# Kernel tuning notes

Measured on AMD Instinct MI355X. Metric: run time of the kernel, lower is better.

The kernel has to match this reference:

```python
import jax, jax.numpy as jnp
import numpy as np

NUM_HEADS = 12


def setup_inputs() -> dict:
    key = jax.random.key(0)
    k1, k2, k3 = jax.random.split(key, 3)
    B, N, C = 4, 2048, 768
    x = jax.random.normal(k1, (B, N, C), dtype=jnp.float32)
    # Linear weights stored as [in, out] so y = x @ W (+ b); matches torch Linear math.
    w_qkv = jax.random.normal(k2, (C, 3 * C), dtype=jnp.float32) * (C ** -0.5)
    w_proj = jax.random.normal(k3, (C, C), dtype=jnp.float32) * (C ** -0.5)
    b_proj = jnp.zeros((C,), dtype=jnp.float32)
    return {"x": x, "w_qkv": w_qkv, "w_proj": w_proj, "b_proj": b_proj}


def reference(x, w_qkv, w_proj, b_proj):
    B, N, C = x.shape
    H = NUM_HEADS
    D = C // H
    scale = D ** -0.5
    qkv = (x @ w_qkv).reshape(B, N, 3, H, D)
    qkv = jnp.transpose(qkv, (2, 0, 3, 1, 4))  # [3, B, H, N, D]
    q, k, v = qkv[0], qkv[1], qkv[2]
    attn = jnp.einsum("bhnd,bhmd->bhnm", q, k) * scale  # [B, H, N, N]
    # causal mask (triu with offset 1), filled with -finfo.max as in the torch code
    causal_mask = jnp.triu(jnp.ones((N, N), dtype=bool), k=1)
    mask_value = -jnp.finfo(attn.dtype).max
    attn = jnp.where(causal_mask, mask_value, attn)
    attn = jax.nn.softmax(attn, axis=-1)
    attn = jnp.nan_to_num(attn)
    out = jnp.einsum("bhnm,bhmd->bhnd", attn, v)  # [B, H, N, D]
    out = jnp.transpose(out, (0, 2, 1, 3)).reshape(B, N, C)
    return out @ w_proj + b_proj
```

## Files before the change

### kernel.cpp

```cpp
#include <hip/hip_runtime.h>
#include <hip/hip_bf16.h>
#include <math.h>

#define BATCH 4
#define SEQ   2048
#define CDIM  768
#define NHEAD 12
#define HDIM  64
#define MROWS (BATCH*SEQ)
#define QKVC  (3*CDIM)

typedef __bf16    bf16x8 __attribute__((ext_vector_type(8)));
typedef _Float16  f16x8  __attribute__((ext_vector_type(8)));
typedef _Float16  f16x4  __attribute__((ext_vector_type(4)));
typedef float     f32x4  __attribute__((ext_vector_type(4)));

__device__ __forceinline__ void async16(const void* g, void* l) {
  __builtin_amdgcn_global_load_lds(
      (const __attribute__((address_space(1))) void*)g,
      (__attribute__((address_space(3))) void*)l, 16, 0, 0);
}

__global__ __launch_bounds__(256) void cast_f32_bf16(
    const float* __restrict__ in, __bf16* __restrict__ out, int n8) {
  int i = blockIdx.x * 256 + threadIdx.x;
  if (i >= n8) return;
  float4 a = reinterpret_cast<const float4*>(in)[i * 2];
  float4 b = reinterpret_cast<const float4*>(in)[i * 2 + 1];
  bf16x8 o;
  o[0] = (__bf16)a.x; o[1] = (__bf16)a.y; o[2] = (__bf16)a.z; o[3] = (__bf16)a.w;
  o[4] = (__bf16)b.x; o[5] = (__bf16)b.y; o[6] = (__bf16)b.z; o[7] = (__bf16)b.w;
  reinterpret_cast<bf16x8*>(out)[i] = o;
}

__global__ __launch_bounds__(256) void transpose_cast(
    const float* __restrict__ w, __bf16* __restrict__ wt, int K, int N) {
  __shared__ float sh[32][33];
  const int n0 = blockIdx.x * 32, k0 = blockIdx.y * 32;
  const int tx = threadIdx.x, ty = threadIdx.y;
#pragma unroll
  for (int i = 0; i < 4; ++i)
    sh[ty + i * 8][tx] = w[(size_t)(k0 + ty + i * 8) * N + n0 + tx];
  __syncthreads();
#pragma unroll
  for (int i = 0; i < 4; ++i)
    wt[(size_t)(n0 + ty + i * 8) * K + k0 + tx] = (__bf16)sh[tx][ty + i * 8];
}

__global__ __launch_bounds__(256) void transpose_v(
    const __bf16* __restrict__ qkv, _Float16* __restrict__ vT) {
  __shared__ float sh[32][33];
  const int c0 = blockIdx.x * 32;
  const int m0 = blockIdx.y * 32;
  const int tx = threadIdx.x, ty = threadIdx.y;
#pragma unroll
  for (int i = 0; i < 4; ++i)
    sh[ty + i * 8][tx] =
        (float)qkv[(size_t)(m0 + ty + i * 8) * QKVC + 2 * CDIM + c0 + tx];
  __syncthreads();
#pragma unroll
  for (int i = 0; i < 4; ++i)
    vT[(size_t)(c0 + ty + i * 8) * MROWS + m0 + tx] = (_Float16)sh[tx][ty + i * 8];
}

template <bool BF16OUT>
__global__ __launch_bounds__(256) void gemm_bf16_kernel(
    const __bf16* __restrict__ A, const __bf16* __restrict__ Bt,
    const float* __restrict__ bias, void* __restrict__ Cout,
    int M, int N, int K) {
  __shared__ __align__(16) __bf16 As[128 * 32];
  __shared__ __align__(16) __bf16 Bs[128 * 32];
  const int tid  = threadIdx.x;
  const int w    = tid >> 6;
  const int lane = tid & 63;
  const int quad = lane >> 4;
  const int lr   = lane & 15;
  const int wr   = w >> 1, wc = w & 1;
  const int mBase = blockIdx.y * 128, nBase = blockIdx.x * 128;

  f32x4 acc[4][4] = {};

  const int srow = lane >> 2;
  const int sk8  = (lane & 3) * 8;
  const __bf16* aSrc0 = A  + (size_t)(mBase + w * 32 + srow) * K + sk8;
  const __bf16* aSrc1 = aSrc0 + (size_t)16 * K;
  const __bf16* bSrc0 = Bt + (size_t)(nBase + w * 32 + srow) * K + sk8;
  const __bf16* bSrc1 = bSrc0 + (size_t)16 * K;
  __bf16* aDst0 = &As[(w * 32 + 0) * 32];
  __bf16* aDst1 = &As[(w * 32 + 16) * 32];
  __bf16* bDst0 = &Bs[(w * 32 + 0) * 32];
  __bf16* bDst1 = &Bs[(w * 32 + 16) * 32];

  for (int k0 = 0; k0 < K; k0 += 32) {
    __syncthreads();
    async16(aSrc0 + k0, aDst0);
    async16(aSrc1 + k0, aDst1);
    async16(bSrc0 + k0, bDst0);
    async16(bSrc1 + k0, bDst1);
    __syncthreads();

    bf16x8 af[4], bfr[4];
#pragma unroll
    for (int mt = 0; mt < 4; ++mt)
      af[mt] = *reinterpret_cast<const bf16x8*>(
          &As[(wr * 64 + mt * 16 + lr) * 32 + quad * 8]);
#pragma unroll
    for (int nt = 0; nt < 4; ++nt)
      bfr[nt] = *reinterpret_cast<const bf16x8*>(
          &Bs[(wc * 64 + nt * 16 + lr) * 32 + quad * 8]);
#pragma unroll
    for (int mt = 0; mt < 4; ++mt)
#pragma unroll
      for (int nt = 0; nt < 4; ++nt)
        acc[mt][nt] = __builtin_amdgcn_mfma_f32_16x16x32_bf16(
            af[mt], bfr[nt], acc[mt][nt], 0, 0, 0);
  }

#pragma unroll
  for (int mt = 0; mt < 4; ++mt) {
#pragma unroll
    for (int nt = 0; nt < 4; ++nt) {
      const int col = nBase + wc * 64 + nt * 16 + lr;
#pragma unroll
      for (int r = 0; r < 4; ++r) {
        const size_t row = (size_t)(mBase + wr * 64 + mt * 16 + quad * 4 + r);
        if (BF16OUT) {
          ((__bf16*)Cout)[row * N + col] = (__bf16)acc[mt][nt][r];
        } else {
          ((float*)Cout)[row * N + col] = acc[mt][nt][r] + bias[col];
        }
      }
    }
  }
}

__global__ __launch_bounds__(256) void flash_mfma_kernel(
    const __bf16* __restrict__ qkv, const _Float16* __restrict__ vT,
    __bf16* __restrict__ out) {
  const int bid = blockIdx.x;
  const int iq  = 31 - (bid / (NHEAD * BATCH));
  const int hb  = bid % (NHEAD * BATCH);
  const int h   = hb % NHEAD;
  const int b   = hb / NHEAD;

  const int tid  = threadIdx.x;
  const int w    = tid >> 6;
  const int lane = tid & 63;
  const int quad = lane >> 4;
  const int lr   = lane & 15;

  __shared__ __align__(16) __bf16   Kf[2][4096];
  __shared__ __align__(16) _Float16 Vf[2][4096];

  bf16x8 qf[2];
  {
    const int qrow = iq * 64 + w * 16 + lr;
    const __bf16* qp = qkv + (size_t)(b * SEQ + qrow) * QKVC + h * HDIM;
    const float qs = 0.125f * 1.44269504088896f;
#pragma unroll
    for (int kc = 0; kc < 2; ++kc) {
      bf16x8 qr = *reinterpret_cast<const bf16x8*>(qp + kc * 32 + quad * 8);
      bf16x8 f;
#pragma unroll
      for (int j = 0; j < 8; ++j) f[j] = (__bf16)((float)qr[j] * qs);
      qf[kc] = f;
    }
  }

  f32x4 O[4];
#pragma unroll
  for (int dt = 0; dt < 4; ++dt) O[dt] = (f32x4){0.f, 0.f, 0.f, 0.f};
  f32x4 O4 = (f32x4){0.f, 0.f, 0.f, 0.f};

  const int sd   = tid >> 2;
  const int sdt  = sd >> 4;
  const int slr  = sd & 15;
  const int snt  = tid & 3;
  const _Float16* vTbase =
      vT + (size_t)(h * HDIM + sd) * MROWS + b * SEQ + snt * 16;

  const __bf16* kSrcBase = qkv + (size_t)(b * SEQ + w * 16 + lr) * QKVC
                           + CDIM + h * HDIM + quad * 8;

#pragma unroll
  for (int kc = 0; kc < 2; ++kc)
    async16(kSrcBase + kc * 32, &Kf[0][(w * 2 + kc) * 512]);
  f16x8 vc0 = *reinterpret_cast<const f16x8*>(vTbase);
  f16x8 vc1 = *reinterpret_cast<const f16x8*>(vTbase + 8);

  int cb = 0;
  for (int kt = 0; kt <= iq; ++kt) {
#pragma unroll
    for (int q = 0; q < 4; ++q) {
      f16x4 val;
#pragma unroll
      for (int j = 0; j < 4; ++j) {
        const int kk = q * 4 + j;
        val[j] = (kk < 8) ? vc0[kk] : vc1[kk - 8];
      }
      *reinterpret_cast<f16x4*>(
          &Vf[cb][(((snt * 4 + sdt) * 64) + q * 16 + slr) * 4]) = val;
    }
    __syncthreads();

    f16x8 vn0, vn1;
    if (kt < iq) {
      const __bf16* ks = kSrcBase + (size_t)(kt + 1) * 64 * QKVC;
#pragma unroll
      for (int kc = 0; kc < 2; ++kc)
        async16(ks + kc * 32, &Kf[cb ^ 1][(w * 2 + kc) * 512]);
      vn0 = *reinterpret_cast<const f16x8*>(vTbase + (size_t)(kt + 1) * 64);
      vn1 = *reinterpret_cast<const f16x8*>(vTbase + (size_t)(kt + 1) * 64 + 8);
    }

    f32x4 s[4];
#pragma unroll
    for (int nt = 0; nt < 4; ++nt) {
      f32x4 acc = (f32x4){0.f, 0.f, 0.f, 0.f};
#pragma unroll
      for (int kc = 0; kc < 2; ++kc) {
        bf16x8 kb = *reinterpret_cast<const bf16x8*>(
            &Kf[cb][((nt * 2 + kc) * 64 + lane) << 3]);
        acc = __builtin_amdgcn_mfma_f32_16x16x32_bf16(kb, qf[kc], acc, 0, 0, 0);
      }
      s[nt] = acc;
    }

    if (kt == iq) {
      const int qg = w * 16 + lr;
#pragma unroll
      for (int nt = 0; nt < 4; ++nt)
#pragma unroll
        for (int r = 0; r < 4; ++r)
          if (nt * 16 + quad * 4 + r > qg) s[nt][r] = -1e30f;
    }

    f16x4 pa[4];
#pragma unroll
    for (int nt = 0; nt < 4; ++nt) {
      f16x4 t;
#pragma unroll
      for (int r = 0; r < 4; ++r)
        t[r] = (_Float16)__builtin_amdgcn_exp2f(s[nt][r]);
      pa[nt] = t;
    }

    const f16x4 vones = {(_Float16)1.f, (_Float16)1.f, (_Float16)1.f, (_Float16)1.f};
#pragma unroll
    for (int nt = 0; nt < 4; ++nt) {
      O4 = __builtin_amdgcn_mfma_f32_16x16x16f16(pa[nt], vones, O4, 0, 0, 0);
#pragma unroll
      for (int dt = 0; dt < 4; ++dt) {
        f16x4 vb = *reinterpret_cast<const f16x4*>(
            &Vf[cb][((nt * 4 + dt) * 64 + lane) * 4]);
        O[dt] = __builtin_amdgcn_mfma_f32_16x16x16f16(pa[nt], vb, O[dt], 0, 0, 0);
      }
    }

    vc0 = vn0; vc1 = vn1;
    cb ^= 1;
  }

  float linv[4];
#pragma unroll
  for (int r = 0; r < 4; ++r) linv[r] = 1.f / O4[r];
  __bf16* obase = out + (size_t)(b * SEQ + iq * 64 + w * 16) * CDIM + h * HDIM;
#pragma unroll
  for (int dt = 0; dt < 4; ++dt)
#pragma unroll
    for (int r = 0; r < 4; ++r)
      obase[(size_t)(quad * 4 + r) * CDIM + dt * 16 + lr] =
          (__bf16)(O[dt][r] * linv[r]);
}

extern "C" void kernel_launch(void* const* d_in, const int* in_sizes, int n_in,
                              void* d_out, int out_size, void* d_ws, size_t ws_size,
                              hipStream_t stream) {
  const float* x      = (const float*)d_in[0];
  const float* w_qkv  = (const float*)d_in[1];
  const float* w_proj = (const float*)d_in[2];
  const float* b_proj = (const float*)d_in[3];
  float* out = (float*)d_out;

  __bf16* qkv    = (__bf16*)d_ws;
  __bf16* attnb  = qkv + (size_t)MROWS * QKVC;
  __bf16* xb     = attnb + (size_t)MROWS * CDIM;
  __bf16* wqkvT  = xb + (size_t)MROWS * CDIM;
  __bf16* wprojT = wqkvT + (size_t)QKVC * CDIM;
  _Float16* vTb  = (_Float16*)(wprojT + (size_t)CDIM * CDIM);

  cast_f32_bf16<<<dim3((MROWS * CDIM / 8 + 255) / 256), dim3(256), 0, stream>>>(
      x, xb, MROWS * CDIM / 8);
  transpose_cast<<<dim3(QKVC / 32, CDIM / 32), dim3(32, 8), 0, stream>>>(
      w_qkv, wqkvT, CDIM, QKVC);
  transpose_cast<<<dim3(CDIM / 32, CDIM / 32), dim3(32, 8), 0, stream>>>(
      w_proj, wprojT, CDIM, CDIM);

  gemm_bf16_kernel<true><<<dim3(QKVC / 128, MROWS / 128), dim3(256), 0, stream>>>(
      xb, wqkvT, nullptr, qkv, MROWS, QKVC, CDIM);

  transpose_v<<<dim3(CDIM / 32, MROWS / 32), dim3(32, 8), 0, stream>>>(qkv, vTb);

  flash_mfma_kernel<<<dim3((SEQ / 64) * NHEAD * BATCH), dim3(256), 0, stream>>>(
      qkv, vTb, attnb);

  gemm_bf16_kernel<false><<<dim3(CDIM / 128, MROWS / 128), dim3(256), 0, stream>>>(
      attnb, wprojT, b_proj, out, MROWS, CDIM, CDIM);
}
```

Before: 214.5 us.

## Pre-swizzle K/V into MFMA fragment layout and give each wave its own query tile

Replaces the V transpose kernel with a swizzle kernel that writes K and V per 64-row tile directly in MFMA fragment order. The flash kernel then drops shared memory and barriers: each wave reads the fragments straight from global/L2 into registers and handles a whole 64-row query tile (4 row groups), so each K/V fragment load feeds 4x more MFMAs. Blocks are remapped so the four waves of a block take different query tiles of one head, balancing causal work, and the grid shrinks to 384 blocks with launch bounds of 2. The cost is much higher register pressure from the larger O accumulators, fewer blocks to fill the device, and relying on cache for K/V reuse between waves.

```diff
diff --git a/kernel.cpp b/kernel.cpp
--- a/kernel.cpp
+++ b/kernel.cpp
@@ -45,22 +45,6 @@
 #pragma unroll
   for (int i = 0; i < 4; ++i)
     wt[(size_t)(n0 + ty + i * 8) * K + k0 + tx] = (__bf16)sh[tx][ty + i * 8];
-}
-
-__global__ __launch_bounds__(256) void transpose_v(
-    const __bf16* __restrict__ qkv, _Float16* __restrict__ vT) {
-  __shared__ float sh[32][33];
-  const int c0 = blockIdx.x * 32;
-  const int m0 = blockIdx.y * 32;
-  const int tx = threadIdx.x, ty = threadIdx.y;
-#pragma unroll
-  for (int i = 0; i < 4; ++i)
-    sh[ty + i * 8][tx] =
-        (float)qkv[(size_t)(m0 + ty + i * 8) * QKVC + 2 * CDIM + c0 + tx];
-  __syncthreads();
-#pragma unroll
-  for (int i = 0; i < 4; ++i)
-    vT[(size_t)(c0 + ty + i * 8) * MROWS + m0 + tx] = (_Float16)sh[tx][ty + i * 8];
 }
 
 template <bool BF16OUT>
@@ -134,143 +118,166 @@
   }
 }
 
-__global__ __launch_bounds__(256) void flash_mfma_kernel(
-    const __bf16* __restrict__ qkv, const _Float16* __restrict__ vT,
-    __bf16* __restrict__ out) {
-  const int bid = blockIdx.x;
-  const int iq  = 31 - (bid / (NHEAD * BATCH));
-  const int hb  = bid % (NHEAD * BATCH);
-  const int h   = hb % NHEAD;
-  const int b   = hb / NHEAD;
-
+__global__ __launch_bounds__(256) void swizzle_kv(
+    const __bf16* __restrict__ qkv, __bf16* __restrict__ kF,
+    _Float16* __restrict__ vF) {
+  const int kt = blockIdx.x;
+  const int hb = blockIdx.y;
+  const int h = hb % NHEAD, b = hb / NHEAD;
+  const int tid = threadIdx.x;
+
+  __shared__ __align__(16) __bf16 Ksh[64][72];
+  __shared__ __align__(16) _Float16 Vsh[64][72];
+
+  const int sr = tid >> 3;
+  const int sc = (tid & 7) * 8;
+  const __bf16* kbase = qkv + (size_t)(b * SEQ + kt * 64) * QKVC + CDIM + h * HDIM;
+  const __bf16* vbase = kbase + CDIM;
+
+#pragma unroll
+  for (int rr = 0; rr < 2; ++rr) {
+    const int row = sr + rr * 32;
+    bf16x8 kv = *reinterpret_cast<const bf16x8*>(kbase + (size_t)row * QKVC + sc);
+    *reinterpret_cast<bf16x8*>(&Ksh[row][sc]) = kv;
+    bf16x8 vv = *reinterpret_cast<const bf16x8*>(vbase + (size_t)row * QKVC + sc);
+    f16x8 vf;
+#pragma unroll
+    for (int j = 0; j < 8; ++j) vf[j] = (_Float16)(float)vv[j];
+    *reinterpret_cast<f16x8*>(&Vsh[row][sc]) = vf;
+  }
+  __syncthreads();
+
+  const size_t tileOff = ((size_t)(hb * 32 + kt)) * 4096;
+
+#pragma unroll
+  for (int ss = 0; ss < 2; ++ss) {
+    const int s = tid + ss * 256;
+    const int f = s >> 6, lane = s & 63;
+    const int nt = f >> 1, kc = f & 1;
+    const int lq = lane >> 4, ll = lane & 15;
+    bf16x8 frag = *reinterpret_cast<const bf16x8*>(
+        &Ksh[nt * 16 + ll][kc * 32 + lq * 8]);
+    *reinterpret_cast<bf16x8*>(&kF[tileOff + (size_t)f * 512 + lane * 8]) = frag;
+  }
+#pragma unroll
+  for (int ss = 0; ss < 2; ++ss) {
+    const int s = tid + ss * 256;
+    const int g = s >> 6, lane = s & 63;
+    const int nt = g >> 1, ph = g & 1;
+    const int lq = lane >> 4, ll = lane & 15;
+    f16x8 frag;
+#pragma unroll
+    for (int j = 0; j < 8; ++j)
+      frag[j] = Vsh[nt * 16 + lq * 4 + (j & 3)][(ph * 2 + (j >> 2)) * 16 + ll];
+    *reinterpret_cast<f16x8*>(&vF[tileOff + (size_t)g * 512 + lane * 8]) = frag;
+  }
+}
+
+__global__ __launch_bounds__(256, 2) void flash_mfma_kernel(
+    const __bf16* __restrict__ qkv, const __bf16* __restrict__ kF,
+    const _Float16* __restrict__ vF, __bf16* __restrict__ out) {
+  const int bid  = blockIdx.x;
   const int tid  = threadIdx.x;
   const int w    = tid >> 6;
   const int lane = tid & 63;
   const int quad = lane >> 4;
   const int lr   = lane & 15;
 
-  __shared__ __align__(16) __bf16   Kf[2][4096];
-  __shared__ __align__(16) _Float16 Vf[2][4096];
-
-  bf16x8 qf[2];
+  const int x   = bid & 7;
+  const int i   = bid >> 3;
+  const int hb  = x * 6 + (i >> 3);
+  const int qt  = 31 - ((i & 7) * 4 + w);
+  const int h   = hb % NHEAD, b = hb / NHEAD;
+
+  bf16x8 qf[4][2];
   {
-    const int qrow = iq * 64 + w * 16 + lr;
-    const __bf16* qp = qkv + (size_t)(b * SEQ + qrow) * QKVC + h * HDIM;
     const float qs = 0.125f * 1.44269504088896f;
-#pragma unroll
-    for (int kc = 0; kc < 2; ++kc) {
-      bf16x8 qr = *reinterpret_cast<const bf16x8*>(qp + kc * 32 + quad * 8);
-      bf16x8 f;
-#pragma unroll
-      for (int j = 0; j < 8; ++j) f[j] = (__bf16)((float)qr[j] * qs);
-      qf[kc] = f;
+    const __bf16* qp = qkv + (size_t)(b * SEQ + qt * 64) * QKVC + h * HDIM;
+#pragma unroll
+    for (int qg = 0; qg < 4; ++qg)
+#pragma unroll
+      for (int kc = 0; kc < 2; ++kc) {
+        bf16x8 qr = *reinterpret_cast<const bf16x8*>(
+            qp + (size_t)(qg * 16 + lr) * QKVC + kc * 32 + quad * 8);
+        bf16x8 f;
+#pragma unroll
+        for (int j = 0; j < 8; ++j) f[j] = (__bf16)((float)qr[j] * qs);
+        qf[qg][kc] = f;
+      }
+  }
+
+  f32x4 O[4][4] = {};
+  f32x4 O4[4] = {};
+
+  const __bf16*   kT = kF + ((size_t)(hb * 32)) * 4096 + lane * 8;
+  const _Float16* vT = vF + ((size_t)(hb * 32)) * 4096 + lane * 8;
+  const f16x4 vones = {(_Float16)1.f, (_Float16)1.f, (_Float16)1.f, (_Float16)1.f};
+
+  for (int kt = 0; kt <= qt; ++kt) {
+    bf16x8 kf[8];
+    f16x8  vf8[8];
+#pragma unroll
+    for (int f = 0; f < 8; ++f)
+      kf[f] = *reinterpret_cast<const bf16x8*>(kT + (size_t)kt * 4096 + f * 512);
+#pragma unroll
+    for (int g = 0; g < 8; ++g)
+      vf8[g] = *reinterpret_cast<const f16x8*>(vT + (size_t)kt * 4096 + g * 512);
+
+#pragma unroll
+    for (int nt = 0; nt < 4; ++nt) {
+      f32x4 s[4];
+#pragma unroll
+      for (int qg = 0; qg < 4; ++qg) {
+        f32x4 acc = (f32x4){0.f, 0.f, 0.f, 0.f};
+        acc = __builtin_amdgcn_mfma_f32_16x16x32_bf16(kf[nt * 2 + 0], qf[qg][0], acc, 0, 0, 0);
+        acc = __builtin_amdgcn_mfma_f32_16x16x32_bf16(kf[nt * 2 + 1], qf[qg][1], acc, 0, 0, 0);
+        s[qg] = acc;
+      }
+      if (kt == qt) {
+#pragma unroll
+        for (int qg = 0; qg < 4; ++qg)
+#pragma unroll
+          for (int r = 0; r < 4; ++r)
+            if (nt * 16 + quad * 4 + r > qg * 16 + lr) s[qg][r] = -1e30f;
+      }
+      f16x4 pa[4];
+#pragma unroll
+      for (int qg = 0; qg < 4; ++qg) {
+        f16x4 t;
+#pragma unroll
+        for (int r = 0; r < 4; ++r)
+          t[r] = (_Float16)__builtin_amdgcn_exp2f(s[qg][r]);
+        pa[qg] = t;
+      }
+#pragma unroll
+      for (int qg = 0; qg < 4; ++qg)
+        O4[qg] = __builtin_amdgcn_mfma_f32_16x16x16f16(pa[qg], vones, O4[qg], 0, 0, 0);
+#pragma unroll
+      for (int dt = 0; dt < 4; ++dt) {
+        const f16x8 vv = vf8[nt * 2 + (dt >> 1)];
+        f16x4 vb;
+#pragma unroll
+        for (int j = 0; j < 4; ++j) vb[j] = vv[(dt & 1) * 4 + j];
+#pragma unroll
+        for (int qg = 0; qg < 4; ++qg)
+          O[qg][dt] = __builtin_amdgcn_mfma_f32_16x16x16f16(pa[qg], vb, O[qg][dt], 0, 0, 0);
+      }
     }
   }
 
-  f32x4 O[4];
-#pragma unroll
-  for (int dt = 0; dt < 4; ++dt) O[dt] = (f32x4){0.f, 0.f, 0.f, 0.f};
-  f32x4 O4 = (f32x4){0.f, 0.f, 0.f, 0.f};
-
-  const int sd   = tid >> 2;
-  const int sdt  = sd >> 4;
-  const int slr  = sd & 15;
-  const int snt  = tid & 3;
-  const _Float16* vTbase =
-      vT + (size_t)(h * HDIM + sd) * MROWS + b * SEQ + snt * 16;
-
-  const __bf16* kSrcBase = qkv + (size_t)(b * SEQ + w * 16 + lr) * QKVC
-                           + CDIM + h * HDIM + quad * 8;
-
-#pragma unroll
-  for (int kc = 0; kc < 2; ++kc)
-    async16(kSrcBase + kc * 32, &Kf[0][(w * 2 + kc) * 512]);
-  f16x8 vc0 = *reinterpret_cast<const f16x8*>(vTbase);
-  f16x8 vc1 = *reinterpret_cast<const f16x8*>(vTbase + 8);
-
-  int cb = 0;
-  for (int kt = 0; kt <= iq; ++kt) {
-#pragma unroll
-    for (int q = 0; q < 4; ++q) {
-      f16x4 val;
-#pragma unroll
-      for (int j = 0; j < 4; ++j) {
-        const int kk = q * 4 + j;
-        val[j] = (kk < 8) ? vc0[kk] : vc1[kk - 8];
-      }
-      *reinterpret_cast<f16x4*>(
-          &Vf[cb][(((snt * 4 + sdt) * 64) + q * 16 + slr) * 4]) = val;
-    }
-    __syncthreads();
-
-    f16x8 vn0, vn1;
-    if (kt < iq) {
-      const __bf16* ks = kSrcBase + (size_t)(kt + 1) * 64 * QKVC;
-#pragma unroll
-      for (int kc = 0; kc < 2; ++kc)
-        async16(ks + kc * 32, &Kf[cb ^ 1][(w * 2 + kc) * 512]);
-      vn0 = *reinterpret_cast<const f16x8*>(vTbase + (size_t)(kt + 1) * 64);
-      vn1 = *reinterpret_cast<const f16x8*>(vTbase + (size_t)(kt + 1) * 64 + 8);
-    }
-
-    f32x4 s[4];
-#pragma unroll
-    for (int nt = 0; nt < 4; ++nt) {
-      f32x4 acc = (f32x4){0.f, 0.f, 0.f, 0.f};
-#pragma unroll
-      for (int kc = 0; kc < 2; ++kc) {
-        bf16x8 kb = *reinterpret_cast<const bf16x8*>(
-            &Kf[cb][((nt * 2 + kc) * 64 + lane) << 3]);
-        acc = __builtin_amdgcn_mfma_f32_16x16x32_bf16(kb, qf[kc], acc, 0, 0, 0);
-      }
-      s[nt] = acc;
-    }
-
-    if (kt == iq) {
-      const int qg = w * 16 + lr;
-#pragma unroll
-      for (int nt = 0; nt < 4; ++nt)
-#pragma unroll
-        for (int r = 0; r < 4; ++r)
-          if (nt * 16 + quad * 4 + r > qg) s[nt][r] = -1e30f;
-    }
-
-    f16x4 pa[4];
-#pragma unroll
-    for (int nt = 0; nt < 4; ++nt) {
-      f16x4 t;
+  __bf16* obase = out + (size_t)(b * SEQ + qt * 64) * CDIM + h * HDIM;
+#pragma unroll
+  for (int qg = 0; qg < 4; ++qg) {
+    float linv[4];
+#pragma unroll
+    for (int r = 0; r < 4; ++r) linv[r] = 1.f / O4[qg][r];
+#pragma unroll
+    for (int dt = 0; dt < 4; ++dt)
 #pragma unroll
       for (int r = 0; r < 4; ++r)
-        t[r] = (_Float16)__builtin_amdgcn_exp2f(s[nt][r]);
-      pa[nt] = t;
-    }
-
-    const f16x4 vones = {(_Float16)1.f, (_Float16)1.f, (_Float16)1.f, (_Float16)1.f};
-#pragma unroll
-    for (int nt = 0; nt < 4; ++nt) {
-      O4 = __builtin_amdgcn_mfma_f32_16x16x16f16(pa[nt], vones, O4, 0, 0, 0);
-#pragma unroll
-      for (int dt = 0; dt < 4; ++dt) {
-        f16x4 vb = *reinterpret_cast<const f16x4*>(
-            &Vf[cb][((nt * 4 + dt) * 64 + lane) * 4]);
-        O[dt] = __builtin_amdgcn_mfma_f32_16x16x16f16(pa[nt], vb, O[dt], 0, 0, 0);
-      }
-    }
-
-    vc0 = vn0; vc1 = vn1;
-    cb ^= 1;
-  }
-
-  float linv[4];
-#pragma unroll
-  for (int r = 0; r < 4; ++r) linv[r] = 1.f / O4[r];
-  __bf16* obase = out + (size_t)(b * SEQ + iq * 64 + w * 16) * CDIM + h * HDIM;
-#pragma unroll
-  for (int dt = 0; dt < 4; ++dt)
-#pragma unroll
-    for (int r = 0; r < 4; ++r)
-      obase[(size_t)(quad * 4 + r) * CDIM + dt * 16 + lr] =
-          (__bf16)(O[dt][r] * linv[r]);
+        obase[(size_t)(qg * 16 + quad * 4 + r) * CDIM + dt * 16 + lr] =
+            (__bf16)(O[qg][dt][r] * linv[r]);
+  }
 }
 
 extern "C" void kernel_launch(void* const* d_in, const int* in_sizes, int n_in,
@@ -287,7 +294,8 @@
   __bf16* xb     = attnb + (size_t)MROWS * CDIM;
   __bf16* wqkvT  = xb + (size_t)MROWS * CDIM;
   __bf16* wprojT = wqkvT + (size_t)QKVC * CDIM;
-  _Float16* vTb  = (_Float16*)(wprojT + (size_t)CDIM * CDIM);
+  __bf16* kFb    = wprojT + (size_t)CDIM * CDIM;
+  _Float16* vFb  = (_Float16*)(kFb + (size_t)48 * 32 * 4096);
 
   cast_f32_bf16<<<dim3((MROWS * CDIM / 8 + 255) / 256), dim3(256), 0, stream>>>(
       x, xb, MROWS * CDIM / 8);
@@ -299,10 +307,9 @@
   gemm_bf16_kernel<true><<<dim3(QKVC / 128, MROWS / 128), dim3(256), 0, stream>>>(
       xb, wqkvT, nullptr, qkv, MROWS, QKVC, CDIM);
 
-  transpose_v<<<dim3(CDIM / 32, MROWS / 32), dim3(32, 8), 0, stream>>>(qkv, vTb);
-
-  flash_mfma_kernel<<<dim3((SEQ / 64) * NHEAD * BATCH), dim3(256), 0, stream>>>(
-      qkv, vTb, attnb);
+  swizzle_kv<<<dim3(32, 48), dim3(256), 0, stream>>>(qkv, kFb, vFb);
+
+  flash_mfma_kernel<<<dim3(384), dim3(256), 0, stream>>>(qkv, kFb, vFb, attnb);
 
   gemm_bf16_kernel<false><<<dim3(CDIM / 128, MROWS / 128), dim3(256), 0, stream>>>(
       attnb, wprojT, b_proj, out, MROWS, CDIM, CDIM);
```

Measured after the change: 239.8 us. 1.12x slower.
